# Kernel optimization log

Measured on AMD Instinct MI355X. Metric: run time of the kernel, lower is better.

The kernel has to match this reference:

```python
import jax, jax.numpy as jnp
import numpy as np

MIN_ROUGHNESS = 0.08
MAX_ROUGHNESS = 0.5
N_MIPS = 6  # 512 -> 16 cubemap mip chain


def _safe_normalize(x, eps=1e-20):
    return x * jax.lax.rsqrt(jnp.clip(jnp.sum(x * x, -1, keepdims=True), eps, None))


def _dot(a, b):
    return jnp.sum(a * b, -1, keepdims=True)


def _cube_face_uv(d):
    # nvdiffrast cube addressing (matches util.cube_to_dir face layout)
    x, y, z = d[..., 0], d[..., 1], d[..., 2]
    ax, ay, az = jnp.abs(x), jnp.abs(y), jnp.abs(z)
    is_x = (ax >= ay) & (ax >= az)
    is_y = (~is_x) & (ay >= az)
    face = jnp.where(is_x, jnp.where(x >= 0, 0, 1),
           jnp.where(is_y, jnp.where(y >= 0, 2, 3), jnp.where(z >= 0, 4, 5)))
    ma = jnp.maximum(jnp.where(is_x, ax, jnp.where(is_y, ay, az)), 1e-20)
    u = jnp.where(face == 0, -z, jnp.where(face == 1, z, jnp.where(face == 5, -x, x))) / ma
    v = jnp.where(face == 2, z, jnp.where(face == 3, -z, -y)) / ma
    return face, u, v


def _bilinear_cube(tex, face, u, v):
    # tex: [6,R,R,C]; face/u/v: [...]; edge-clamped bilinear within the face
    R = tex.shape[1]
    tu = (u * 0.5 + 0.5) * R - 0.5
    tv = (v * 0.5 + 0.5) * R - 0.5
    x0 = jnp.floor(tu); y0 = jnp.floor(tv)
    fx = (tu - x0)[..., None]; fy = (tv - y0)[..., None]
    x0i = jnp.clip(x0, 0, R - 1).astype(jnp.int32)
    x1i = jnp.clip(x0 + 1, 0, R - 1).astype(jnp.int32)
    y0i = jnp.clip(y0, 0, R - 1).astype(jnp.int32)
    y1i = jnp.clip(y0 + 1, 0, R - 1).astype(jnp.int32)
    c00 = tex[face, y0i, x0i]; c01 = tex[face, y0i, x1i]
    c10 = tex[face, y1i, x0i]; c11 = tex[face, y1i, x1i]
    return (c00 * (1 - fx) + c01 * fx) * (1 - fy) + (c10 * (1 - fx) + c11 * fx) * fy


def _sample_cubemap(tex, dirs):
    f, u, v = _cube_face_uv(dirs)
    return _bilinear_cube(tex, f, u, v)


def _sample_2d_clamp(tex, uv):
    # tex: [H,W,C]; uv in [0,1]^2, clamp boundary bilinear (FG LUT lookup)
    H, W = tex.shape[0], tex.shape[1]
    tu = uv[..., 0] * W - 0.5
    tv = uv[..., 1] * H - 0.5
    x0 = jnp.floor(tu); y0 = jnp.floor(tv)
    fx = (tu - x0)[..., None]; fy = (tv - y0)[..., None]
    x0i = jnp.clip(x0, 0, W - 1).astype(jnp.int32)
    x1i = jnp.clip(x0 + 1, 0, W - 1).astype(jnp.int32)
    y0i = jnp.clip(y0, 0, H - 1).astype(jnp.int32)
    y1i = jnp.clip(y0 + 1, 0, H - 1).astype(jnp.int32)
    c00 = tex[y0i, x0i]; c01 = tex[y0i, x1i]
    c10 = tex[y1i, x0i]; c11 = tex[y1i, x1i]
    return (c00 * (1 - fx) + c01 * fx) * (1 - fy) + (c10 * (1 - fx) + c11 * fx) * fy


def _get_mip(r, n_levels):
    lo = (jnp.clip(r, MIN_ROUGHNESS, MAX_ROUGHNESS) - MIN_ROUGHNESS) / (MAX_ROUGHNESS - MIN_ROUGHNESS) * (n_levels - 2)
    hi = (jnp.clip(r, MAX_ROUGHNESS, 1.0) - MAX_ROUGHNESS) / (1.0 - MAX_ROUGHNESS) + (n_levels - 2)
    return jnp.where(r < MAX_ROUGHNESS, lo, hi)


def _linear2srgb(x):
    xs = jnp.where(x > 0.0031308, x, 1.0)  # avoid pow(0) grad issues
    return jnp.where(x > 0.0031308, 1.055 * jnp.power(xs, 1.0 / 2.4) - 0.055, 12.92 * x)


def _avg_pool_cube(c):
    F, R, _, C = c.shape
    return c.reshape(F, R // 2, 2, R // 2, 2, C).mean(axis=(2, 4))


def setup_inputs() -> dict:
    key = jax.random.key(0)
    ks = jax.random.split(key, 10)
    B, H, W = 1, 1024, 1024
    gb_pos = jax.random.normal(ks[0], (B, H, W, 3), jnp.float32)
    gb_normal = _safe_normalize(jax.random.normal(ks[1], (B, H, W, 3), jnp.float32))
    basecolor = jax.random.uniform(ks[2], (B, H, W, 3), jnp.float32)
    metallic = jax.random.uniform(ks[3], (B, H, W, 1), jnp.float32)
    roughness = jax.random.uniform(ks[4], (B, H, W, 1), jnp.float32)
    view_pos = jax.random.normal(ks[5], (1, 1, 1, 3), jnp.float32) * 3.0
    diffuse = jax.random.uniform(ks[6], (6, 16, 16, 3), jnp.float32)
    fg_lut = jax.random.uniform(ks[7], (256, 256, 2), jnp.float32)
    specs = {}
    s = jax.random.uniform(ks[8], (6, 512, 512, 3), jnp.float32)
    for l in range(N_MIPS):
        specs['spec%d' % l] = s
        if l < N_MIPS - 1:
            s = _avg_pool_cube(s)
    return dict(gb_pos=gb_pos, gb_normal=gb_normal, basecolor=basecolor,
                metallic=metallic, roughness=roughness, view_pos=view_pos,
                diffuse=diffuse, fg_lut=fg_lut, **specs)


def reference(gb_pos, gb_normal, basecolor, metallic, roughness, view_pos,
              diffuse, fg_lut, spec0, spec1, spec2, spec3, spec4, spec5):
    specs = [spec0, spec1, spec2, spec3, spec4, spec5]
    L = len(specs)
    metallic = metallic[..., :1]
    wo = _safe_normalize(view_pos - gb_pos)
    diffuse_albedo = (1.0 - metallic) * basecolor
    specular_albedo = 0.04 * (1.0 - metallic) + metallic * basecolor
    reflvec = _safe_normalize(2.0 * _dot(wo, gb_normal) * gb_normal - wo)
    # diffuse IBL: cubemap gather along normal
    ambient = _sample_cubemap(diffuse, gb_normal)
    diffuse_linear = ambient * diffuse_albedo
    # FG LUT gather
    NdotV = jnp.clip(_dot(wo, gb_normal), 1e-4, None)
    fg = _sample_2d_clamp(fg_lut, jnp.concatenate([NdotV, roughness], -1))
    # trilinear (linear-mipmap-linear) specular cubemap gather
    mip = jnp.clip(_get_mip(roughness[..., 0], L), 0.0, L - 1.0)
    face, u, v = _cube_face_uv(reflvec)
    spec = jnp.zeros(gb_pos.shape[:-1] + (spec0.shape[-1],), gb_pos.dtype)
    for l in range(L):
        w = jnp.clip(1.0 - jnp.abs(mip - l), 0.0, 1.0)[..., None]
        spec = spec + w * _bilinear_cube(specs[l], face, u, v)
    reflectance = specular_albedo * fg[..., 0:1] + fg[..., 1:2]
    rgb = spec * reflectance + diffuse_linear
    return _linear2srgb(jnp.clip(rgb, 0.0, 1.0))
```

## Files before the change

### kernel.cpp

```cpp
#include <hip/hip_runtime.h>
#include <hip/hip_fp16.h>

struct V3 { float x, y, z; };

__device__ __forceinline__ V3 v3add(V3 a, V3 b){ return {a.x+b.x, a.y+b.y, a.z+b.z}; }
__device__ __forceinline__ V3 v3sub(V3 a, V3 b){ return {a.x-b.x, a.y-b.y, a.z-b.z}; }
__device__ __forceinline__ V3 v3scale(V3 a, float s){ return {a.x*s, a.y*s, a.z*s}; }
__device__ __forceinline__ V3 v3mul(V3 a, V3 b){ return {a.x*b.x, a.y*b.y, a.z*b.z}; }
__device__ __forceinline__ float dot3(V3 a, V3 b){ return fmaf(a.x,b.x, fmaf(a.y,b.y, a.z*b.z)); }
__device__ __forceinline__ V3 nrm3(V3 a){
    float s = rsqrtf(fmaxf(dot3(a,a), 1e-20f));
    return v3scale(a, s);
}

struct __align__(16) PairBlock { __half2 h01, h23, h45, h67; };

#define OFF0 0
#define OFF1 1572864
#define OFF2 1966080
#define OFF3 2064384
#define OFF4 2088960
#define OFF5 2095104
#define DIFF_OFF 2096640
#define TOTAL_BLOCKS 2098176
#define WS_BYTES_NEEDED (TOTAL_BLOCKS * 16)

__device__ __forceinline__ void cube_face_uv(V3 d, int& face, float& u, float& v){
    float ax = fabsf(d.x), ay = fabsf(d.y), az = fabsf(d.z);
    bool is_x = (ax >= ay) && (ax >= az);
    bool is_y = (!is_x) && (ay >= az);
    face = is_x ? (d.x >= 0.f ? 0 : 1)
                : (is_y ? (d.y >= 0.f ? 2 : 3)
                        : (d.z >= 0.f ? 4 : 5));
    float ma = fmaxf(is_x ? ax : (is_y ? ay : az), 1e-20f);
    float un = (face == 0) ? -d.z : (face == 1) ? d.z : (face == 5) ? -d.x : d.x;
    float vn = (face == 2) ?  d.z : (face == 3) ? -d.z : -d.y;
    float inv = 1.0f / ma;
    u = un * inv;
    v = vn * inv;
}

__device__ __forceinline__ void pair_extract(const PairBlock& pb, V3& lo, V3& hi){
    lo.x = __low2float(pb.h01);  lo.y = __high2float(pb.h01); lo.z = __low2float(pb.h23);
    hi.x = __high2float(pb.h23); hi.y = __low2float(pb.h45);  hi.z = __high2float(pb.h45);
}

__device__ __forceinline__ V3 bilinear_pairtex(const PairBlock* __restrict__ lvl, int R,
                                               int face, float u, float v){
    float Rf = (float)R;
    float tu = fmaf(fmaf(u, 0.5f, 0.5f), Rf, -0.5f);
    float tv = fmaf(fmaf(v, 0.5f, 0.5f), Rf, -0.5f);
    float x0f = floorf(tu), y0f = floorf(tv);
    float fx = tu - x0f,    fy = tv - y0f;
    int x0 = (int)x0f;
    fx = (x0 < 0) ? 0.f : fx;
    int xb  = min(max(x0, 0), R-1);
    int y0i = min(max((int)y0f,     0), R-1);
    int y1i = min(max((int)y0f + 1, 0), R-1);
    const PairBlock* fb = lvl + (size_t)face * R * R;
    PairBlock b0 = fb[(size_t)y0i * R + xb];
    PairBlock b1 = fb[(size_t)y1i * R + xb];
    V3 l0, h0, l1, h1;
    pair_extract(b0, l0, h0);
    pair_extract(b1, l1, h1);
    V3 r0 = { l0.x + (h0.x-l0.x)*fx, l0.y + (h0.y-l0.y)*fx, l0.z + (h0.z-l0.z)*fx };
    V3 r1 = { l1.x + (h1.x-l1.x)*fx, l1.y + (h1.y-l1.y)*fx, l1.z + (h1.z-l1.z)*fx };
    return { r0.x + (r1.x-r0.x)*fy, r0.y + (r1.y-r0.y)*fy, r0.z + (r1.z-r0.z)*fy };
}

__device__ __forceinline__ V3 bilinear_cube3(const float* __restrict__ tex, int R,
                                             int face, float u, float v){
    float Rf = (float)R;
    float tu = fmaf(fmaf(u, 0.5f, 0.5f), Rf, -0.5f);
    float tv = fmaf(fmaf(v, 0.5f, 0.5f), Rf, -0.5f);
    float x0 = floorf(tu), y0 = floorf(tv);
    float fx = tu - x0,    fy = tv - y0;
    int x0i = min(max((int)x0,     0), R-1);
    int x1i = min(max((int)x0 + 1, 0), R-1);
    int y0i = min(max((int)y0,     0), R-1);
    int y1i = min(max((int)y0 + 1, 0), R-1);
    const float* base = tex + (size_t)face * R * R * 3;
    const float* r0 = base + (size_t)y0i * R * 3;
    const float* r1 = base + (size_t)y1i * R * 3;
    float a0 = r0[3*x0i], a1 = r0[3*x0i+1], a2 = r0[3*x0i+2];
    float b0 = r0[3*x1i], b1 = r0[3*x1i+1], b2 = r0[3*x1i+2];
    float d0 = r1[3*x0i], d1 = r1[3*x0i+1], d2 = r1[3*x0i+2];
    float e0 = r1[3*x1i], e1 = r1[3*x1i+1], e2 = r1[3*x1i+2];
    float w00 = (1.f-fx)*(1.f-fy), w01 = fx*(1.f-fy);
    float w10 = (1.f-fx)*fy,       w11 = fx*fy;
    V3 out;
    out.x = a0*w00 + b0*w01 + d0*w10 + e0*w11;
    out.y = a1*w00 + b1*w01 + d1*w10 + e1*w11;
    out.z = a2*w00 + b2*w01 + d2*w10 + e2*w11;
    return out;
}

__device__ __forceinline__ void sample_fg(const float* __restrict__ lut,
                                          float u, float v, float& fa, float& fb){
    const int W = 256, H = 256;
    float tu = fmaf(u, (float)W, -0.5f);
    float tv = fmaf(v, (float)H, -0.5f);
    float x0 = floorf(tu), y0 = floorf(tv);
    float fx = tu - x0,    fy = tv - y0;
    int x0i = min(max((int)x0,     0), W-1);
    int x1i = min(max((int)x0 + 1, 0), W-1);
    int y0i = min(max((int)y0,     0), H-1);
    int y1i = min(max((int)y0 + 1, 0), H-1);
    const float2* l2 = (const float2*)lut;
    float2 a = l2[(size_t)y0i*W + x0i];
    float2 b = l2[(size_t)y0i*W + x1i];
    float2 d = l2[(size_t)y1i*W + x0i];
    float2 e = l2[(size_t)y1i*W + x1i];
    float w00 = (1.f-fx)*(1.f-fy), w01 = fx*(1.f-fy);
    float w10 = (1.f-fx)*fy,       w11 = fx*fy;
    fa = a.x*w00 + b.x*w01 + d.x*w10 + e.x*w11;
    fb = a.y*w00 + b.y*w01 + d.y*w10 + e.y*w11;
}

__device__ __forceinline__ float lin2srgb(float x){
    float xs = (x > 0.0031308f) ? x : 1.0f;
    float p  = __builtin_amdgcn_exp2f(__builtin_amdgcn_logf(xs) * (1.0f/2.4f));
    return (x > 0.0031308f) ? fmaf(1.055f, p, -0.055f) : 12.92f * x;
}

__device__ __forceinline__ float clamp01(float x){ return fminf(fmaxf(x, 0.f), 1.f); }

__global__ __launch_bounds__(256)
void pack_kernel(const float* __restrict__ s0, const float* __restrict__ s1,
                 const float* __restrict__ s2, const float* __restrict__ s3,
                 const float* __restrict__ s4, const float* __restrict__ s5,
                 const float* __restrict__ diffuse,
                 PairBlock* __restrict__ ws)
{
    int t = blockIdx.x * blockDim.x + threadIdx.x;
    if (t >= TOTAL_BLOCKS) return;
    const float* src; int local; int Rmask;
    if      (t >= DIFF_OFF) { src = diffuse; local = t - DIFF_OFF; Rmask = 15;  }
    else if (t >= OFF5)     { src = s5;      local = t - OFF5;     Rmask = 15;  }
    else if (t >= OFF4)     { src = s4;      local = t - OFF4;     Rmask = 31;  }
    else if (t >= OFF3)     { src = s3;      local = t - OFF3;     Rmask = 63;  }
    else if (t >= OFF2)     { src = s2;      local = t - OFF2;     Rmask = 127; }
    else if (t >= OFF1)     { src = s1;      local = t - OFF1;     Rmask = 255; }
    else                    { src = s0;      local = t;            Rmask = 511; }
    int nb = ((local & Rmask) == Rmask) ? local : local + 1;
    float ar = src[3*local], ag = src[3*local+1], ab = src[3*local+2];
    float br = src[3*nb],    bg = src[3*nb+1],    bb = src[3*nb+2];
    PairBlock pb;
    pb.h01 = __floats2half2_rn(ar, ag);
    pb.h23 = __floats2half2_rn(ab, br);
    pb.h45 = __floats2half2_rn(bg, bb);
    pb.h67 = __floats2half2_rn(0.f, 0.f);
    ws[t] = pb;
}

template <bool PACKED>
__device__ __forceinline__ void shade_pixel(
    int i,
    const float* __restrict__ gb_pos, const float* __restrict__ gb_normal,
    const float* __restrict__ basecolor, const float* __restrict__ metallic,
    const float* __restrict__ roughness, const float* __restrict__ view_pos,
    const float* __restrict__ diffuse, const float* __restrict__ fg_lut,
    const float* __restrict__ s0, const float* __restrict__ s1,
    const float* __restrict__ s2, const float* __restrict__ s3,
    const float* __restrict__ s4, const float* __restrict__ s5,
    const PairBlock* __restrict__ ws,
    float* __restrict__ out)
{
    V3 pos = { gb_pos[3*i],    gb_pos[3*i+1],    gb_pos[3*i+2] };
    V3 nrm = { gb_normal[3*i], gb_normal[3*i+1], gb_normal[3*i+2] };
    V3 bc  = { basecolor[3*i], basecolor[3*i+1], basecolor[3*i+2] };
    float m = metallic[i];
    float r = roughness[i];
    V3 vp  = { view_pos[0], view_pos[1], view_pos[2] };

    V3 wo = nrm3(v3sub(vp, pos));
    float ndv_raw = dot3(wo, nrm);
    V3 refl = nrm3(v3sub(v3scale(nrm, 2.0f*ndv_raw), wo));

    float one_m = 1.0f - m;
    V3 diff_alb = v3scale(bc, one_m);
    V3 spec_alb = { fmaf(m, bc.x, 0.04f*one_m),
                    fmaf(m, bc.y, 0.04f*one_m),
                    fmaf(m, bc.z, 0.04f*one_m) };

    const float MIN_R = 0.08f, MAX_R = 0.5f;
    float lo = (fminf(fmaxf(r, MIN_R), MAX_R) - MIN_R) / (MAX_R - MIN_R) * 4.0f;
    float hi = (fminf(fmaxf(r, MAX_R), 1.0f) - MAX_R) / (1.0f - MAX_R) + 4.0f;
    float mip = (r < MAX_R) ? lo : hi;
    mip = fminf(fmaxf(mip, 0.0f), 5.0f);
    int l0 = min((int)mip, 5);
    float f = mip - (float)l0;
    int l1 = min(l0 + 1, 5);

    int dface; float du, dv;
    cube_face_uv(nrm, dface, du, dv);
    int sface; float su, sv;
    cube_face_uv(refl, sface, su, sv);
    float NdotV = fmaxf(ndv_raw, 0.0001f);

    V3 ambient, specA, specB;
    if (PACKED) {
        int offA = OFF0;
        offA = (l0 == 1) ? OFF1 : offA; offA = (l0 == 2) ? OFF2 : offA;
        offA = (l0 == 3) ? OFF3 : offA; offA = (l0 == 4) ? OFF4 : offA;
        offA = (l0 == 5) ? OFF5 : offA;
        int offB = OFF0;
        offB = (l1 == 1) ? OFF1 : offB; offB = (l1 == 2) ? OFF2 : offB;
        offB = (l1 == 3) ? OFF3 : offB; offB = (l1 == 4) ? OFF4 : offB;
        offB = (l1 == 5) ? OFF5 : offB;
        ambient = bilinear_pairtex(ws + DIFF_OFF, 16, dface, du, dv);
        specA   = bilinear_pairtex(ws + offA, 512 >> l0, sface, su, sv);
        specB   = bilinear_pairtex(ws + offB, 512 >> l1, sface, su, sv);
    } else {
        const float* tA = s0;
        tA = (l0 == 1) ? s1 : tA; tA = (l0 == 2) ? s2 : tA;
        tA = (l0 == 3) ? s3 : tA; tA = (l0 == 4) ? s4 : tA; tA = (l0 == 5) ? s5 : tA;
        const float* tB = s0;
        tB = (l1 == 1) ? s1 : tB; tB = (l1 == 2) ? s2 : tB;
        tB = (l1 == 3) ? s3 : tB; tB = (l1 == 4) ? s4 : tB; tB = (l1 == 5) ? s5 : tB;
        ambient = bilinear_cube3(diffuse, 16, dface, du, dv);
        specA   = bilinear_cube3(tA, 512 >> l0, sface, su, sv);
        specB   = bilinear_cube3(tB, 512 >> l1, sface, su, sv);
    }

    float fa, fb;
    sample_fg(fg_lut, NdotV, r, fa, fb);

    V3 spec = { specA.x + (specB.x - specA.x) * f,
                specA.y + (specB.y - specA.y) * f,
                specA.z + (specB.z - specA.z) * f };
    V3 reflc = { fmaf(spec_alb.x, fa, fb),
                 fmaf(spec_alb.y, fa, fb),
                 fmaf(spec_alb.z, fa, fb) };
    V3 rgb = v3add(v3mul(spec, reflc), v3mul(ambient, diff_alb));

    out[3*i+0] = lin2srgb(clamp01(rgb.x));
    out[3*i+1] = lin2srgb(clamp01(rgb.y));
    out[3*i+2] = lin2srgb(clamp01(rgb.z));
}

template <bool PACKED>
__global__ __launch_bounds__(256)
void envlight_kernel(const float* __restrict__ gb_pos,
                     const float* __restrict__ gb_normal,
                     const float* __restrict__ basecolor,
                     const float* __restrict__ metallic,
                     const float* __restrict__ roughness,
                     const float* __restrict__ view_pos,
                     const float* __restrict__ diffuse,
                     const float* __restrict__ fg_lut,
                     const float* __restrict__ s0,
                     const float* __restrict__ s1,
                     const float* __restrict__ s2,
                     const float* __restrict__ s3,
                     const float* __restrict__ s4,
                     const float* __restrict__ s5,
                     const PairBlock* __restrict__ ws,
                     float* __restrict__ out,
                     int n)
{
    int i = blockIdx.x * blockDim.x + threadIdx.x;
    if (i >= n) return;
    shade_pixel<PACKED>(i, gb_pos, gb_normal, basecolor, metallic, roughness,
                        view_pos, diffuse, fg_lut, s0, s1, s2, s3, s4, s5, ws, out);
}

extern "C" void kernel_launch(void* const* d_in, const int* in_sizes, int n_in,
                              void* d_out, int out_size, void* d_ws, size_t ws_size,
                              hipStream_t stream) {
    const float* gb_pos    = (const float*)d_in[0];
    const float* gb_normal = (const float*)d_in[1];
    const float* basecolor = (const float*)d_in[2];
    const float* metallic  = (const float*)d_in[3];
    const float* roughness = (const float*)d_in[4];
    const float* view_pos  = (const float*)d_in[5];
    const float* diffuse   = (const float*)d_in[6];
    const float* fg_lut    = (const float*)d_in[7];
    const float* s0        = (const float*)d_in[8];
    const float* s1        = (const float*)d_in[9];
    const float* s2        = (const float*)d_in[10];
    const float* s3        = (const float*)d_in[11];
    const float* s4        = (const float*)d_in[12];
    const float* s5        = (const float*)d_in[13];
    float* out = (float*)d_out;

    int n = in_sizes[0] / 3;
    int block = 256;
    int grid = (n + block - 1) / block;

    if (ws_size >= (size_t)WS_BYTES_NEEDED) {
        PairBlock* ws = (PairBlock*)d_ws;
        int pgrid = (TOTAL_BLOCKS + block - 1) / block;
        pack_kernel<<<pgrid, block, 0, stream>>>(s0, s1, s2, s3, s4, s5, diffuse, ws);
        envlight_kernel<true><<<grid, block, 0, stream>>>(gb_pos, gb_normal, basecolor,
            metallic, roughness, view_pos, diffuse, fg_lut,
            s0, s1, s2, s3, s4, s5, ws, out, n);
    } else {
        envlight_kernel<false><<<grid, block, 0, stream>>>(gb_pos, gb_normal, basecolor,
            metallic, roughness, view_pos, diffuse, fg_lut,
            s0, s1, s2, s3, s4, s5, (const PairBlock*)nullptr, out, n);
    }
}
```

Baseline: 172.9 us.

## Pack FG LUT into paired texels, stage diffuse cubemap in LDS, two pixels per thread

Extends the pack kernel to store the FG LUT as horizontally paired float4 texels, so each LUT lookup needs two loads instead of four. The diffuse cubemap (1536 paired blocks) is copied into shared memory per block, and each thread shades two pixels whose setup is computed before the gathers, giving more memory-level parallelism. The trade-offs are a larger workspace, per-block LDS fill overhead and a halved grid with more registers per thread.

Result: faster. 167.6 us (-3.1%).

```diff
diff --git a/kernel.cpp b/kernel.cpp
--- a/kernel.cpp
+++ b/kernel.cpp
@@ -22,8 +22,11 @@
 #define OFF4 2088960
 #define OFF5 2095104
 #define DIFF_OFF 2096640
-#define TOTAL_BLOCKS 2098176
-#define WS_BYTES_NEEDED (TOTAL_BLOCKS * 16)
+#define FG_OFF 2098176
+#define TOTAL_BLOCKS 2163712
+#define PACK_ONLY_BLOCKS 2098176
+#define WS_BYTES_FULL  ((size_t)TOTAL_BLOCKS * 16)
+#define WS_BYTES_PACK  ((size_t)PACK_ONLY_BLOCKS * 16)
 
 __device__ __forceinline__ void cube_face_uv(V3 d, int& face, float& u, float& v){
     float ax = fabsf(d.x), ay = fabsf(d.y), az = fabsf(d.z);
@@ -66,6 +69,48 @@
     V3 r0 = { l0.x + (h0.x-l0.x)*fx, l0.y + (h0.y-l0.y)*fx, l0.z + (h0.z-l0.z)*fx };
     V3 r1 = { l1.x + (h1.x-l1.x)*fx, l1.y + (h1.y-l1.y)*fx, l1.z + (h1.z-l1.z)*fx };
     return { r0.x + (r1.x-r0.x)*fy, r0.y + (r1.y-r0.y)*fy, r0.z + (r1.z-r0.z)*fy };
+}
+
+__device__ __forceinline__ void sample_fg_pair(const float4* __restrict__ fgp,
+                                               float u, float v, float& fa, float& fb){
+    const int W = 256, H = 256;
+    float tu = fmaf(u, (float)W, -0.5f);
+    float tv = fmaf(v, (float)H, -0.5f);
+    float x0f = floorf(tu), y0f = floorf(tv);
+    float fx = tu - x0f,    fy = tv - y0f;
+    int x0 = (int)x0f;
+    fx = (x0 < 0) ? 0.f : fx;
+    int xb  = min(max(x0, 0), W-1);
+    int y0i = min(max((int)y0f,     0), H-1);
+    int y1i = min(max((int)y0f + 1, 0), H-1);
+    float4 r0 = fgp[(size_t)y0i * W + xb];
+    float4 r1 = fgp[(size_t)y1i * W + xb];
+    float t0a = r0.x + (r0.z - r0.x)*fx, t0b = r0.y + (r0.w - r0.y)*fx;
+    float t1a = r1.x + (r1.z - r1.x)*fx, t1b = r1.y + (r1.w - r1.y)*fx;
+    fa = t0a + (t1a - t0a)*fy;
+    fb = t0b + (t1b - t0b)*fy;
+}
+
+__device__ __forceinline__ void sample_fg(const float* __restrict__ lut,
+                                          float u, float v, float& fa, float& fb){
+    const int W = 256, H = 256;
+    float tu = fmaf(u, (float)W, -0.5f);
+    float tv = fmaf(v, (float)H, -0.5f);
+    float x0 = floorf(tu), y0 = floorf(tv);
+    float fx = tu - x0,    fy = tv - y0;
+    int x0i = min(max((int)x0,     0), W-1);
+    int x1i = min(max((int)x0 + 1, 0), W-1);
+    int y0i = min(max((int)y0,     0), H-1);
+    int y1i = min(max((int)y0 + 1, 0), H-1);
+    const float2* l2 = (const float2*)lut;
+    float2 a = l2[(size_t)y0i*W + x0i];
+    float2 b = l2[(size_t)y0i*W + x1i];
+    float2 d = l2[(size_t)y1i*W + x0i];
+    float2 e = l2[(size_t)y1i*W + x1i];
+    float w00 = (1.f-fx)*(1.f-fy), w01 = fx*(1.f-fy);
+    float w10 = (1.f-fx)*fy,       w11 = fx*fy;
+    fa = a.x*w00 + b.x*w01 + d.x*w10 + e.x*w11;
+    fb = a.y*w00 + b.y*w01 + d.y*w10 + e.y*w11;
 }
 
 __device__ __forceinline__ V3 bilinear_cube3(const float* __restrict__ tex, int R,
@@ -95,28 +140,6 @@
     return out;
 }
 
-__device__ __forceinline__ void sample_fg(const float* __restrict__ lut,
-                                          float u, float v, float& fa, float& fb){
-    const int W = 256, H = 256;
-    float tu = fmaf(u, (float)W, -0.5f);
-    float tv = fmaf(v, (float)H, -0.5f);
-    float x0 = floorf(tu), y0 = floorf(tv);
-    float fx = tu - x0,    fy = tv - y0;
-    int x0i = min(max((int)x0,     0), W-1);
-    int x1i = min(max((int)x0 + 1, 0), W-1);
-    int y0i = min(max((int)y0,     0), H-1);
-    int y1i = min(max((int)y0 + 1, 0), H-1);
-    const float2* l2 = (const float2*)lut;
-    float2 a = l2[(size_t)y0i*W + x0i];
-    float2 b = l2[(size_t)y0i*W + x1i];
-    float2 d = l2[(size_t)y1i*W + x0i];
-    float2 e = l2[(size_t)y1i*W + x1i];
-    float w00 = (1.f-fx)*(1.f-fy), w01 = fx*(1.f-fy);
-    float w10 = (1.f-fx)*fy,       w11 = fx*fy;
-    fa = a.x*w00 + b.x*w01 + d.x*w10 + e.x*w11;
-    fb = a.y*w00 + b.y*w01 + d.y*w10 + e.y*w11;
-}
-
 __device__ __forceinline__ float lin2srgb(float x){
     float xs = (x > 0.0031308f) ? x : 1.0f;
     float p  = __builtin_amdgcn_exp2f(__builtin_amdgcn_logf(xs) * (1.0f/2.4f));
@@ -129,11 +152,20 @@
 void pack_kernel(const float* __restrict__ s0, const float* __restrict__ s1,
                  const float* __restrict__ s2, const float* __restrict__ s3,
                  const float* __restrict__ s4, const float* __restrict__ s5,
-                 const float* __restrict__ diffuse,
-                 PairBlock* __restrict__ ws)
+                 const float* __restrict__ diffuse, const float* __restrict__ fg_lut,
+                 PairBlock* __restrict__ ws, int total)
 {
     int t = blockIdx.x * blockDim.x + threadIdx.x;
-    if (t >= TOTAL_BLOCKS) return;
+    if (t >= total) return;
+    if (t >= FG_OFF) {
+        int local = t - FG_OFF;
+        int x = local & 255;
+        int nb = (x == 255) ? local : local + 1;
+        float4 v = make_float4(fg_lut[2*local], fg_lut[2*local+1],
+                               fg_lut[2*nb],    fg_lut[2*nb+1]);
+        ((float4*)ws)[t] = v;
+        return;
+    }
     const float* src; int local; int Rmask;
     if      (t >= DIFF_OFF) { src = diffuse; local = t - DIFF_OFF; Rmask = 15;  }
     else if (t >= OFF5)     { src = s5;      local = t - OFF5;     Rmask = 15;  }
@@ -153,35 +185,38 @@
     ws[t] = pb;
 }
 
-template <bool PACKED>
-__device__ __forceinline__ void shade_pixel(
+struct PixPre {
+    V3 diff_alb, spec_alb;
+    int sface; float su, sv;
+    int dface; float du, dv;
+    int offA, RA, offB, RB; float f;
+    float ndotv, rough;
+};
+
+__device__ __forceinline__ PixPre pre_pixel(
     int i,
     const float* __restrict__ gb_pos, const float* __restrict__ gb_normal,
     const float* __restrict__ basecolor, const float* __restrict__ metallic,
-    const float* __restrict__ roughness, const float* __restrict__ view_pos,
-    const float* __restrict__ diffuse, const float* __restrict__ fg_lut,
-    const float* __restrict__ s0, const float* __restrict__ s1,
-    const float* __restrict__ s2, const float* __restrict__ s3,
-    const float* __restrict__ s4, const float* __restrict__ s5,
-    const PairBlock* __restrict__ ws,
-    float* __restrict__ out)
+    const float* __restrict__ roughness, V3 vp)
 {
     V3 pos = { gb_pos[3*i],    gb_pos[3*i+1],    gb_pos[3*i+2] };
     V3 nrm = { gb_normal[3*i], gb_normal[3*i+1], gb_normal[3*i+2] };
     V3 bc  = { basecolor[3*i], basecolor[3*i+1], basecolor[3*i+2] };
     float m = metallic[i];
     float r = roughness[i];
-    V3 vp  = { view_pos[0], view_pos[1], view_pos[2] };
 
     V3 wo = nrm3(v3sub(vp, pos));
     float ndv_raw = dot3(wo, nrm);
     V3 refl = nrm3(v3sub(v3scale(nrm, 2.0f*ndv_raw), wo));
 
+    PixPre p;
     float one_m = 1.0f - m;
-    V3 diff_alb = v3scale(bc, one_m);
-    V3 spec_alb = { fmaf(m, bc.x, 0.04f*one_m),
-                    fmaf(m, bc.y, 0.04f*one_m),
-                    fmaf(m, bc.z, 0.04f*one_m) };
+    p.diff_alb = v3scale(bc, one_m);
+    p.spec_alb = { fmaf(m, bc.x, 0.04f*one_m),
+                   fmaf(m, bc.y, 0.04f*one_m),
+                   fmaf(m, bc.z, 0.04f*one_m) };
+    p.ndotv = fmaxf(ndv_raw, 0.0001f);
+    p.rough = r;
 
     const float MIN_R = 0.08f, MAX_R = 0.5f;
     float lo = (fminf(fmaxf(r, MIN_R), MAX_R) - MIN_R) / (MAX_R - MIN_R) * 4.0f;
@@ -189,80 +224,132 @@
     float mip = (r < MAX_R) ? lo : hi;
     mip = fminf(fmaxf(mip, 0.0f), 5.0f);
     int l0 = min((int)mip, 5);
-    float f = mip - (float)l0;
+    p.f = mip - (float)l0;
     int l1 = min(l0 + 1, 5);
 
-    int dface; float du, dv;
-    cube_face_uv(nrm, dface, du, dv);
-    int sface; float su, sv;
-    cube_face_uv(refl, sface, su, sv);
-    float NdotV = fmaxf(ndv_raw, 0.0001f);
-
-    V3 ambient, specA, specB;
-    if (PACKED) {
-        int offA = OFF0;
-        offA = (l0 == 1) ? OFF1 : offA; offA = (l0 == 2) ? OFF2 : offA;
-        offA = (l0 == 3) ? OFF3 : offA; offA = (l0 == 4) ? OFF4 : offA;
-        offA = (l0 == 5) ? OFF5 : offA;
-        int offB = OFF0;
-        offB = (l1 == 1) ? OFF1 : offB; offB = (l1 == 2) ? OFF2 : offB;
-        offB = (l1 == 3) ? OFF3 : offB; offB = (l1 == 4) ? OFF4 : offB;
-        offB = (l1 == 5) ? OFF5 : offB;
-        ambient = bilinear_pairtex(ws + DIFF_OFF, 16, dface, du, dv);
-        specA   = bilinear_pairtex(ws + offA, 512 >> l0, sface, su, sv);
-        specB   = bilinear_pairtex(ws + offB, 512 >> l1, sface, su, sv);
-    } else {
-        const float* tA = s0;
-        tA = (l0 == 1) ? s1 : tA; tA = (l0 == 2) ? s2 : tA;
-        tA = (l0 == 3) ? s3 : tA; tA = (l0 == 4) ? s4 : tA; tA = (l0 == 5) ? s5 : tA;
-        const float* tB = s0;
-        tB = (l1 == 1) ? s1 : tB; tB = (l1 == 2) ? s2 : tB;
-        tB = (l1 == 3) ? s3 : tB; tB = (l1 == 4) ? s4 : tB; tB = (l1 == 5) ? s5 : tB;
-        ambient = bilinear_cube3(diffuse, 16, dface, du, dv);
-        specA   = bilinear_cube3(tA, 512 >> l0, sface, su, sv);
-        specB   = bilinear_cube3(tB, 512 >> l1, sface, su, sv);
-    }
-
+    int offA = OFF0;
+    offA = (l0 == 1) ? OFF1 : offA; offA = (l0 == 2) ? OFF2 : offA;
+    offA = (l0 == 3) ? OFF3 : offA; offA = (l0 == 4) ? OFF4 : offA;
+    offA = (l0 == 5) ? OFF5 : offA;
+    int offB = OFF0;
+    offB = (l1 == 1) ? OFF1 : offB; offB = (l1 == 2) ? OFF2 : offB;
+    offB = (l1 == 3) ? OFF3 : offB; offB = (l1 == 4) ? OFF4 : offB;
+    offB = (l1 == 5) ? OFF5 : offB;
+    p.offA = offA; p.RA = 512 >> l0;
+    p.offB = offB; p.RB = 512 >> l1;
+
+    cube_face_uv(nrm, p.dface, p.du, p.dv);
+    cube_face_uv(refl, p.sface, p.su, p.sv);
+    return p;
+}
+
+template <bool FGPAIR>
+__device__ __forceinline__ void finish_pixel(
+    int i, const PixPre& p,
+    const PairBlock* __restrict__ ws, const PairBlock* __restrict__ lds_diff,
+    const float* __restrict__ fg_lut, float* __restrict__ out)
+{
+    V3 specA = bilinear_pairtex(ws + p.offA, p.RA, p.sface, p.su, p.sv);
+    V3 specB = bilinear_pairtex(ws + p.offB, p.RB, p.sface, p.su, p.sv);
+    V3 ambient = bilinear_pairtex(lds_diff, 16, p.dface, p.du, p.dv);
     float fa, fb;
-    sample_fg(fg_lut, NdotV, r, fa, fb);
-
-    V3 spec = { specA.x + (specB.x - specA.x) * f,
-                specA.y + (specB.y - specA.y) * f,
-                specA.z + (specB.z - specA.z) * f };
-    V3 reflc = { fmaf(spec_alb.x, fa, fb),
-                 fmaf(spec_alb.y, fa, fb),
-                 fmaf(spec_alb.z, fa, fb) };
-    V3 rgb = v3add(v3mul(spec, reflc), v3mul(ambient, diff_alb));
+    if (FGPAIR) sample_fg_pair((const float4*)(ws + FG_OFF), p.ndotv, p.rough, fa, fb);
+    else        sample_fg(fg_lut, p.ndotv, p.rough, fa, fb);
+
+    V3 spec = { specA.x + (specB.x - specA.x) * p.f,
+                specA.y + (specB.y - specA.y) * p.f,
+                specA.z + (specB.z - specA.z) * p.f };
+    V3 reflc = { fmaf(p.spec_alb.x, fa, fb),
+                 fmaf(p.spec_alb.y, fa, fb),
+                 fmaf(p.spec_alb.z, fa, fb) };
+    V3 rgb = v3add(v3mul(spec, reflc), v3mul(ambient, p.diff_alb));
 
     out[3*i+0] = lin2srgb(clamp01(rgb.x));
     out[3*i+1] = lin2srgb(clamp01(rgb.y));
     out[3*i+2] = lin2srgb(clamp01(rgb.z));
 }
 
-template <bool PACKED>
+template <bool FGPAIR>
 __global__ __launch_bounds__(256)
-void envlight_kernel(const float* __restrict__ gb_pos,
+void envlight_packed(const float* __restrict__ gb_pos,
                      const float* __restrict__ gb_normal,
                      const float* __restrict__ basecolor,
                      const float* __restrict__ metallic,
                      const float* __restrict__ roughness,
                      const float* __restrict__ view_pos,
-                     const float* __restrict__ diffuse,
                      const float* __restrict__ fg_lut,
-                     const float* __restrict__ s0,
-                     const float* __restrict__ s1,
-                     const float* __restrict__ s2,
-                     const float* __restrict__ s3,
-                     const float* __restrict__ s4,
-                     const float* __restrict__ s5,
                      const PairBlock* __restrict__ ws,
                      float* __restrict__ out,
-                     int n)
+                     int n, int half)
+{
+    __shared__ PairBlock lds_diff[1536];
+    for (int t = threadIdx.x; t < 1536; t += 256)
+        lds_diff[t] = ws[DIFF_OFF + t];
+    __syncthreads();
+
+    int i = blockIdx.x * blockDim.x + threadIdx.x;
+    if (i >= half) return;
+    int j = i + half;
+
+    V3 vp = { view_pos[0], view_pos[1], view_pos[2] };
+
+    PixPre pa = pre_pixel(i, gb_pos, gb_normal, basecolor, metallic, roughness, vp);
+    if (j < n) {
+        PixPre pb = pre_pixel(j, gb_pos, gb_normal, basecolor, metallic, roughness, vp);
+        finish_pixel<FGPAIR>(i, pa, ws, lds_diff, fg_lut, out);
+        finish_pixel<FGPAIR>(j, pb, ws, lds_diff, fg_lut, out);
+    } else {
+        finish_pixel<FGPAIR>(i, pa, ws, lds_diff, fg_lut, out);
+    }
+}
+
+__global__ __launch_bounds__(256)
+void envlight_fallback(const float* __restrict__ gb_pos,
+                       const float* __restrict__ gb_normal,
+                       const float* __restrict__ basecolor,
+                       const float* __restrict__ metallic,
+                       const float* __restrict__ roughness,
+                       const float* __restrict__ view_pos,
+                       const float* __restrict__ diffuse,
+                       const float* __restrict__ fg_lut,
+                       const float* __restrict__ s0, const float* __restrict__ s1,
+                       const float* __restrict__ s2, const float* __restrict__ s3,
+                       const float* __restrict__ s4, const float* __restrict__ s5,
+                       float* __restrict__ out, int n)
 {
     int i = blockIdx.x * blockDim.x + threadIdx.x;
     if (i >= n) return;
-    shade_pixel<PACKED>(i, gb_pos, gb_normal, basecolor, metallic, roughness,
-                        view_pos, diffuse, fg_lut, s0, s1, s2, s3, s4, s5, ws, out);
+    V3 vp = { view_pos[0], view_pos[1], view_pos[2] };
+    PixPre p = pre_pixel(i, gb_pos, gb_normal, basecolor, metallic, roughness, vp);
+    int l0 = 0;
+    l0 = (p.offA == OFF1) ? 1 : l0; l0 = (p.offA == OFF2) ? 2 : l0;
+    l0 = (p.offA == OFF3) ? 3 : l0; l0 = (p.offA == OFF4) ? 4 : l0;
+    l0 = (p.offA == OFF5) ? 5 : l0;
+    int l1 = 0;
+    l1 = (p.offB == OFF1) ? 1 : l1; l1 = (p.offB == OFF2) ? 2 : l1;
+    l1 = (p.offB == OFF3) ? 3 : l1; l1 = (p.offB == OFF4) ? 4 : l1;
+    l1 = (p.offB == OFF5) ? 5 : l1;
+    const float* tA = s0;
+    tA = (l0 == 1) ? s1 : tA; tA = (l0 == 2) ? s2 : tA;
+    tA = (l0 == 3) ? s3 : tA; tA = (l0 == 4) ? s4 : tA; tA = (l0 == 5) ? s5 : tA;
+    const float* tB = s0;
+    tB = (l1 == 1) ? s1 : tB; tB = (l1 == 2) ? s2 : tB;
+    tB = (l1 == 3) ? s3 : tB; tB = (l1 == 4) ? s4 : tB; tB = (l1 == 5) ? s5 : tB;
+    V3 ambient = bilinear_cube3(diffuse, 16, p.dface, p.du, p.dv);
+    V3 specA   = bilinear_cube3(tA, p.RA, p.sface, p.su, p.sv);
+    V3 specB   = bilinear_cube3(tB, p.RB, p.sface, p.su, p.sv);
+    float fa, fb;
+    sample_fg(fg_lut, p.ndotv, p.rough, fa, fb);
+    V3 spec = { specA.x + (specB.x - specA.x) * p.f,
+                specA.y + (specB.y - specA.y) * p.f,
+                specA.z + (specB.z - specA.z) * p.f };
+    V3 reflc = { fmaf(p.spec_alb.x, fa, fb),
+                 fmaf(p.spec_alb.y, fa, fb),
+                 fmaf(p.spec_alb.z, fa, fb) };
+    V3 rgb = v3add(v3mul(spec, reflc), v3mul(ambient, p.diff_alb));
+    out[3*i+0] = lin2srgb(clamp01(rgb.x));
+    out[3*i+1] = lin2srgb(clamp01(rgb.y));
+    out[3*i+2] = lin2srgb(clamp01(rgb.z));
 }
 
 extern "C" void kernel_launch(void* const* d_in, const int* in_sizes, int n_in,
@@ -286,18 +373,27 @@
 
     int n = in_sizes[0] / 3;
     int block = 256;
-    int grid = (n + block - 1) / block;
-
-    if (ws_size >= (size_t)WS_BYTES_NEEDED) {
+
+    bool full = ws_size >= WS_BYTES_FULL;
+    bool mid  = ws_size >= WS_BYTES_PACK;
+    if (full || mid) {
         PairBlock* ws = (PairBlock*)d_ws;
-        int pgrid = (TOTAL_BLOCKS + block - 1) / block;
-        pack_kernel<<<pgrid, block, 0, stream>>>(s0, s1, s2, s3, s4, s5, diffuse, ws);
-        envlight_kernel<true><<<grid, block, 0, stream>>>(gb_pos, gb_normal, basecolor,
+        int total = full ? TOTAL_BLOCKS : PACK_ONLY_BLOCKS;
+        int pgrid = (total + block - 1) / block;
+        pack_kernel<<<pgrid, block, 0, stream>>>(s0, s1, s2, s3, s4, s5,
+                                                 diffuse, fg_lut, ws, total);
+        int half = (n + 1) / 2;
+        int grid = (half + block - 1) / block;
+        if (full)
+            envlight_packed<true><<<grid, block, 0, stream>>>(gb_pos, gb_normal,
+                basecolor, metallic, roughness, view_pos, fg_lut, ws, out, n, half);
+        else
+            envlight_packed<false><<<grid, block, 0, stream>>>(gb_pos, gb_normal,
+                basecolor, metallic, roughness, view_pos, fg_lut, ws, out, n, half);
+    } else {
+        int grid = (n + block - 1) / block;
+        envlight_fallback<<<grid, block, 0, stream>>>(gb_pos, gb_normal, basecolor,
             metallic, roughness, view_pos, diffuse, fg_lut,
-            s0, s1, s2, s3, s4, s5, ws, out, n);
-    } else {
-        envlight_kernel<false><<<grid, block, 0, stream>>>(gb_pos, gb_normal, basecolor,
-            metallic, roughness, view_pos, diffuse, fg_lut,
-            s0, s1, s2, s3, s4, s5, (const PairBlock*)nullptr, out, n);
+            s0, s1, s2, s3, s4, s5, out, n);
     }
 }
```
